# Kernel optimization log

Hardware: AMD Instinct MI355X
Metric: run time of the kernel (lower is better)

## Reference

```python
import jax, jax.numpy as jnp
import numpy as np

ITERS = 10
EPS = 1e-6
TEMPERATURE = 1.0


def setup_inputs() -> dict:
    key = jax.random.key(0)
    S, E = 524288, 64
    logits = jax.random.normal(key, (S, E), dtype=jnp.float32)
    return {"logits": logits, "top_k": 2}


def reference(logits, top_k):
    s, e = logits.shape
    scores = (logits / TEMPERATURE).astype(jnp.float32)
    scores = scores - jnp.max(scores, axis=-1, keepdims=True)
    q = jnp.exp(scores)
    col_target = float(s) / float(max(e, 1))

    def body(q, _):
        q = q / (jnp.sum(q, axis=1, keepdims=True) + EPS)
        q = q / (jnp.sum(q, axis=0, keepdims=True) + EPS) * col_target
        return q, None

    q, _ = jax.lax.scan(body, q, None, length=ITERS)
    q = q / (jnp.sum(q, axis=1, keepdims=True) + EPS)
    vals, idx = jax.lax.top_k(q, top_k)
    w = vals / (jnp.sum(vals, axis=-1, keepdims=True) + EPS)
    return idx.astype(jnp.int64), w.astype(logits.dtype)
```

## Files before the change

kernel.cpp:

```cpp
#include <hip/hip_runtime.h>
#include <math.h>

#define EPS 1e-6f
#define NE 64
#define TPB 1024
#define WPB 16
#define NBLK 256
#define NWAVES (NBLK * WPB)
#define ITERS 10
#define PF 4

template <int ctrl>
__device__ __forceinline__ float dppf(float x) {
    return __int_as_float(__builtin_amdgcn_update_dpp(
        0, __float_as_int(x), ctrl, 0xf, 0xf, true));
}
template <int ctrl>
__device__ __forceinline__ int dppi(int x) {
    return __builtin_amdgcn_update_dpp(0, x, ctrl, 0xf, 0xf, true);
}

__device__ __forceinline__ float group16_sum(float v) {
    v += dppf<0xB1>(v);
    v += dppf<0x4E>(v);
    v += dppf<0x141>(v);
    v += dppf<0x140>(v);
    return v;
}

#define ARGMAX_STEP(CTRL)                                      \
    {                                                          \
        float ov = dppf<CTRL>(v);                              \
        int oi = dppi<CTRL>(i);                                \
        if (ov > v || (ov == v && oi < i)) { v = ov; i = oi; } \
    }

__device__ __forceinline__ void group16_argmax(float& v, int& i) {
    ARGMAX_STEP(0xB1)
    ARGMAX_STEP(0x4E)
    ARGMAX_STEP(0x141)
    ARGMAX_STEP(0x140)
}

__global__ __launch_bounds__(TPB, 4) void sink_fused(
    const float4* __restrict__ logits4,
    float* __restrict__ Pblk,
    unsigned* __restrict__ counters,
    float2* __restrict__ oidx, float2* __restrict__ ow,
    int nquads, float col_target) {
    __shared__ float4 plds[WPB][64];
    __shared__ float s_red[16][NE];
    __shared__ float r_lds[WPB * 128];
    __shared__ float4 c_lds4[NE / 4];

    const int tid = threadIdx.x;
    const int lane = tid & 63;
    const int wib = tid >> 6;
    const int g = lane >> 4;
    const int h = lane & 15;
    const int qpw = nquads / NWAVES;
    const int qbase = (blockIdx.x * WPB + wib) * qpw;
    const float4* lp = logits4 + (size_t)qbase * 64 + lane;
    const int nb = qpw / PF;
    const int lrow0 = wib * 128 + g;

    if (tid < NE / 4) c_lds4[tid] = make_float4(1.f, 1.f, 1.f, 1.f);
    __syncthreads();

    for (int it = 0; it < ITERS; ++it) {
        const float4 c4 = c_lds4[h];
        float* Pcur = Pblk + (size_t)(it & 1) * NBLK * NE;

        float4 buf[PF];
#pragma unroll
        for (int p = 0; p < PF; ++p) buf[p] = lp[(size_t)p * 64];

        float4 pacc = {0.f, 0.f, 0.f, 0.f};
        for (int b = 0; b < nb; ++b) {
            float4 cur[PF];
#pragma unroll
            for (int p = 0; p < PF; ++p) cur[p] = buf[p];
            if (b + 1 < nb) {
                const float4* np = lp + (size_t)(b + 1) * PF * 64;
#pragma unroll
                for (int p = 0; p < PF; ++p) buf[p] = np[(size_t)p * 64];
            }
#pragma unroll
            for (int p = 0; p < PF; ++p) {
                float4 q;
                q.x = __expf(cur[p].x); q.y = __expf(cur[p].y);
                q.z = __expf(cur[p].z); q.w = __expf(cur[p].w);
                float s = q.x * c4.x + q.y * c4.y + q.z * c4.z + q.w * c4.w;
                s = group16_sum(s);
                const int lrow = lrow0 + (b * PF + p) * 4;
                float rold = (it == 0) ? 1.0f : r_lds[lrow];
                float rnew = rold / (rold * s + EPS);
                if (h == 0) r_lds[lrow] = rnew;
                pacc.x += q.x * rnew; pacc.y += q.y * rnew;
                pacc.z += q.z * rnew; pacc.w += q.w * rnew;
            }
        }

        plds[wib][lane] = pacc;
        __syncthreads();
        if (tid < NE) {
            const int hh = tid >> 2, kk = tid & 3;
            float t = 0.f;
#pragma unroll
            for (int w = 0; w < WPB; ++w)
#pragma unroll
                for (int gg = 0; gg < 4; ++gg)
                    t += ((const float*)&plds[w][gg * 16 + hh])[kk];
            __hip_atomic_store(&Pcur[blockIdx.x * NE + tid], t,
                               __ATOMIC_RELAXED, __HIP_MEMORY_SCOPE_AGENT);
        }
        __syncthreads();

        if (tid == 0) {
            __builtin_amdgcn_fence(__ATOMIC_RELEASE, "agent");
            __hip_atomic_fetch_add(&counters[it], 1u, __ATOMIC_RELAXED,
                                   __HIP_MEMORY_SCOPE_AGENT);
            while (__hip_atomic_load(&counters[it], __ATOMIC_RELAXED,
                                     __HIP_MEMORY_SCOPE_AGENT) < (unsigned)NBLK)
                __builtin_amdgcn_s_sleep(2);
            __builtin_amdgcn_fence(__ATOMIC_ACQUIRE, "agent");
        }
        __syncthreads();

        {
            const int col = tid & 63;
            const int chunk = tid >> 6;
            const int b0 = chunk * (NBLK / 16);
            float t = 0.f;
#pragma unroll
            for (int b2 = 0; b2 < NBLK / 16; ++b2)
                t += __hip_atomic_load(&Pcur[(b0 + b2) * NE + col],
                                       __ATOMIC_RELAXED,
                                       __HIP_MEMORY_SCOPE_AGENT);
            s_red[chunk][col] = t;
        }
        __syncthreads();
        if (tid < NE) {
            float P = 0.f;
#pragma unroll
            for (int k = 0; k < 16; ++k) P += s_red[k][tid];
            float cj = ((float*)c_lds4)[tid];
            ((float*)c_lds4)[tid] = cj * col_target / (cj * P + EPS);
        }
        __syncthreads();
    }

    {
        const float4 c4 = c_lds4[h];
        const int base_col = h * 4;

        float4 buf[PF];
#pragma unroll
        for (int p = 0; p < PF; ++p) buf[p] = lp[(size_t)p * 64];

        for (int b = 0; b < nb; ++b) {
            float4 cur[PF];
#pragma unroll
            for (int p = 0; p < PF; ++p) cur[p] = buf[p];
            if (b + 1 < nb) {
                const float4* np = lp + (size_t)(b + 1) * PF * 64;
#pragma unroll
                for (int p = 0; p < PF; ++p) buf[p] = np[(size_t)p * 64];
            }
#pragma unroll
            for (int p = 0; p < PF; ++p) {
                float4 u;
                u.x = __expf(cur[p].x) * c4.x; u.y = __expf(cur[p].y) * c4.y;
                u.z = __expf(cur[p].z) * c4.z; u.w = __expf(cur[p].w) * c4.w;
                float s = group16_sum(u.x + u.y + u.z + u.w);
                const int lrow = lrow0 + (b * PF + p) * 4;
                float rold = r_lds[lrow];
                float rnew = rold / (rold * s + EPS);
                float4 val;
                val.x = u.x * rnew; val.y = u.y * rnew;
                val.z = u.z * rnew; val.w = u.w * rnew;

                float v = val.x; int i = base_col;
                if (val.y > v) { v = val.y; i = base_col + 1; }
                if (val.z > v) { v = val.z; i = base_col + 2; }
                if (val.w > v) { v = val.w; i = base_col + 3; }
                group16_argmax(v, i);
                float v1 = v; int i1 = i;

                float4 mv;
                mv.x = (i1 == base_col)     ? -INFINITY : val.x;
                mv.y = (i1 == base_col + 1) ? -INFINITY : val.y;
                mv.z = (i1 == base_col + 2) ? -INFINITY : val.z;
                mv.w = (i1 == base_col + 3) ? -INFINITY : val.w;
                v = mv.x; i = base_col;
                if (mv.y > v) { v = mv.y; i = base_col + 1; }
                if (mv.z > v) { v = mv.z; i = base_col + 2; }
                if (mv.w > v) { v = mv.w; i = base_col + 3; }
                group16_argmax(v, i);
                float v2 = v; int i2 = i;

                if (h == 0) {
                    int row = (qbase + b * PF + p) * 4 + g;
                    float wsum = v1 + v2 + EPS;
                    oidx[row] = make_float2((float)i1, (float)i2);
                    ow[row] = make_float2(v1 / wsum, v2 / wsum);
                }
            }
        }
    }
}

extern "C" void kernel_launch(void* const* d_in, const int* in_sizes, int n_in,
                              void* d_out, int out_size, void* d_ws, size_t ws_size,
                              hipStream_t stream) {
    const float* logits = (const float*)d_in[0];
    const int S = in_sizes[0] / NE;
    const int nquads = S / 4;
    const float col_target = (float)S / (float)NE;

    float* Pblk = (float*)d_ws;
    unsigned* counters = (unsigned*)(Pblk + 2 * NBLK * NE);

    float* out = (float*)d_out;
    float2* oidx = (float2*)out;
    float2* ow = (float2*)(out + (size_t)2 * S);

    hipMemsetAsync(counters, 0, ITERS * sizeof(unsigned), stream);
    sink_fused<<<NBLK, TPB, 0, stream>>>((const float4*)logits, Pblk, counters,
                                         oidx, ow, nquads, col_target);
}
```

Measured before the change: 555.9 us.

## Deepen prefetch to 8 quads and carry prefetched loads across iteration barriers

Doubles the per-wave software prefetch depth from 4 to 8 float4 loads and rotates the buffer slot by slot, so each slot is refilled right after it is consumed. The last batch of each pass wraps around to prefetch the first batch of the next pass, so loads for the next iteration are in flight during the grid-wide barrier and column reduction. This aims to hide global-memory latency and the per-pass restart bubble. The cost is more VGPRs per thread, which under launch_bounds(1024,4) could cause spills.

```diff
diff --git a/kernel.cpp b/kernel.cpp
--- a/kernel.cpp
+++ b/kernel.cpp
@@ -8,7 +8,7 @@
 #define NBLK 256
 #define NWAVES (NBLK * WPB)
 #define ITERS 10
-#define PF 4
+#define PF 8
 
 template <int ctrl>
 __device__ __forceinline__ float dppf(float x) {
@@ -65,31 +65,27 @@
     const int lrow0 = wib * 128 + g;
 
     if (tid < NE / 4) c_lds4[tid] = make_float4(1.f, 1.f, 1.f, 1.f);
+
+    float4 buf[PF];
+#pragma unroll
+    for (int p = 0; p < PF; ++p) buf[p] = lp[(size_t)p * 64];
     __syncthreads();
 
     for (int it = 0; it < ITERS; ++it) {
         const float4 c4 = c_lds4[h];
         float* Pcur = Pblk + (size_t)(it & 1) * NBLK * NE;
 
-        float4 buf[PF];
-#pragma unroll
-        for (int p = 0; p < PF; ++p) buf[p] = lp[(size_t)p * 64];
-
         float4 pacc = {0.f, 0.f, 0.f, 0.f};
         for (int b = 0; b < nb; ++b) {
-            float4 cur[PF];
-#pragma unroll
-            for (int p = 0; p < PF; ++p) cur[p] = buf[p];
-            if (b + 1 < nb) {
-                const float4* np = lp + (size_t)(b + 1) * PF * 64;
-#pragma unroll
-                for (int p = 0; p < PF; ++p) buf[p] = np[(size_t)p * 64];
-            }
+            const int nxt = (b + 1 < nb) ? (b + 1) * PF : 0;
+            const float4* np = lp + (size_t)nxt * 64;
 #pragma unroll
             for (int p = 0; p < PF; ++p) {
+                const float4 cur = buf[p];
+                buf[p] = np[(size_t)p * 64];
                 float4 q;
-                q.x = __expf(cur[p].x); q.y = __expf(cur[p].y);
-                q.z = __expf(cur[p].z); q.w = __expf(cur[p].w);
+                q.x = __expf(cur.x); q.y = __expf(cur.y);
+                q.z = __expf(cur.z); q.w = __expf(cur.w);
                 float s = q.x * c4.x + q.y * c4.y + q.z * c4.z + q.w * c4.w;
                 s = group16_sum(s);
                 const int lrow = lrow0 + (b * PF + p) * 4;
@@ -154,24 +150,16 @@
         const float4 c4 = c_lds4[h];
         const int base_col = h * 4;
 
-        float4 buf[PF];
-#pragma unroll
-        for (int p = 0; p < PF; ++p) buf[p] = lp[(size_t)p * 64];
-
         for (int b = 0; b < nb; ++b) {
-            float4 cur[PF];
-#pragma unroll
-            for (int p = 0; p < PF; ++p) cur[p] = buf[p];
-            if (b + 1 < nb) {
-                const float4* np = lp + (size_t)(b + 1) * PF * 64;
-#pragma unroll
-                for (int p = 0; p < PF; ++p) buf[p] = np[(size_t)p * 64];
-            }
+            const bool more = (b + 1 < nb);
+            const float4* np = lp + (size_t)(b + 1) * PF * 64;
 #pragma unroll
             for (int p = 0; p < PF; ++p) {
+                const float4 cur = buf[p];
+                if (more) buf[p] = np[(size_t)p * 64];
                 float4 u;
-                u.x = __expf(cur[p].x) * c4.x; u.y = __expf(cur[p].y) * c4.y;
-                u.z = __expf(cur[p].z) * c4.z; u.w = __expf(cur[p].w) * c4.w;
+                u.x = __expf(cur.x) * c4.x; u.y = __expf(cur.y) * c4.y;
+                u.z = __expf(cur.z) * c4.z; u.w = __expf(cur.w) * c4.w;
                 float s = group16_sum(u.x + u.y + u.z + u.w);
                 const int lrow = lrow0 + (b * PF + p) * 4;
                 float rold = r_lds[lrow];
```

Measured after the change: 537.3 us. -3.3%, faster.

## Cache exponentiated logits in registers and LDS across Sinkhorn iterations

Applied to the files above, without the earlier changes.

Each wave's 32 row-quads of exp(logits) are now computed once. The first 16 are kept in registers and the next 8 in dynamic LDS. Only the last 8 are reloaded from global memory and re-exponentiated on each iteration and in the final top-2 pass. This removes most of the repeated 128MB global reads and exp work per iteration. In exchange, register pressure rises, 128KB of dynamic LDS is needed, QPW is hardcoded to 32 so the kernel only handles this problem size, and the occupancy hint is dropped.

```diff
diff --git a/kernel.cpp b/kernel.cpp
--- a/kernel.cpp
+++ b/kernel.cpp
@@ -8,7 +8,10 @@
 #define NBLK 256
 #define NWAVES (NBLK * WPB)
 #define ITERS 10
-#define PF 4
+#define QPW 32
+#define NR 16
+#define NL 8
+#define NS 8
 
 template <int ctrl>
 __device__ __forceinline__ float dppf(float x) {
@@ -42,12 +45,13 @@
     ARGMAX_STEP(0x140)
 }
 
-__global__ __launch_bounds__(TPB, 4) void sink_fused(
+__global__ __launch_bounds__(TPB) void sink_fused(
     const float4* __restrict__ logits4,
     float* __restrict__ Pblk,
     unsigned* __restrict__ counters,
     float2* __restrict__ oidx, float2* __restrict__ ow,
     int nquads, float col_target) {
+    extern __shared__ float4 ldsq[];
     __shared__ float4 plds[WPB][64];
     __shared__ float s_red[16][NE];
     __shared__ float r_lds[WPB * 128];
@@ -58,49 +62,34 @@
     const int wib = tid >> 6;
     const int g = lane >> 4;
     const int h = lane & 15;
-    const int qpw = nquads / NWAVES;
-    const int qbase = (blockIdx.x * WPB + wib) * qpw;
+    const int qbase = (blockIdx.x * WPB + wib) * QPW;
     const float4* lp = logits4 + (size_t)qbase * 64 + lane;
-    const int nb = qpw / PF;
     const int lrow0 = wib * 128 + g;
 
     if (tid < NE / 4) c_lds4[tid] = make_float4(1.f, 1.f, 1.f, 1.f);
     __syncthreads();
 
-    for (int it = 0; it < ITERS; ++it) {
-        const float4 c4 = c_lds4[h];
+    auto exp4 = [](const float4& v) {
+        float4 e;
+        e.x = __expf(v.x); e.y = __expf(v.y);
+        e.z = __expf(v.z); e.w = __expf(v.w);
+        return e;
+    };
+
+    auto procq = [&](const float4& e, int q, const float4& c4, float4& pacc,
+                     bool first) {
+        float s = e.x * c4.x + e.y * c4.y + e.z * c4.z + e.w * c4.w;
+        s = group16_sum(s);
+        const int lrow = lrow0 + q * 4;
+        float rold = first ? 1.0f : r_lds[lrow];
+        float rnew = rold / (rold * s + EPS);
+        if (h == 0) r_lds[lrow] = rnew;
+        pacc.x += e.x * rnew; pacc.y += e.y * rnew;
+        pacc.z += e.z * rnew; pacc.w += e.w * rnew;
+    };
+
+    auto col_reduce_barrier = [&](const float4& pacc, int it) {
         float* Pcur = Pblk + (size_t)(it & 1) * NBLK * NE;
-
-        float4 buf[PF];
-#pragma unroll
-        for (int p = 0; p < PF; ++p) buf[p] = lp[(size_t)p * 64];
-
-        float4 pacc = {0.f, 0.f, 0.f, 0.f};
-        for (int b = 0; b < nb; ++b) {
-            float4 cur[PF];
-#pragma unroll
-            for (int p = 0; p < PF; ++p) cur[p] = buf[p];
-            if (b + 1 < nb) {
-                const float4* np = lp + (size_t)(b + 1) * PF * 64;
-#pragma unroll
-                for (int p = 0; p < PF; ++p) buf[p] = np[(size_t)p * 64];
-            }
-#pragma unroll
-            for (int p = 0; p < PF; ++p) {
-                float4 q;
-                q.x = __expf(cur[p].x); q.y = __expf(cur[p].y);
-                q.z = __expf(cur[p].z); q.w = __expf(cur[p].w);
-                float s = q.x * c4.x + q.y * c4.y + q.z * c4.z + q.w * c4.w;
-                s = group16_sum(s);
-                const int lrow = lrow0 + (b * PF + p) * 4;
-                float rold = (it == 0) ? 1.0f : r_lds[lrow];
-                float rnew = rold / (rold * s + EPS);
-                if (h == 0) r_lds[lrow] = rnew;
-                pacc.x += q.x * rnew; pacc.y += q.y * rnew;
-                pacc.z += q.z * rnew; pacc.w += q.w * rnew;
-            }
-        }
-
         plds[wib][lane] = pacc;
         __syncthreads();
         if (tid < NE) {
@@ -115,7 +104,6 @@
                                __ATOMIC_RELAXED, __HIP_MEMORY_SCOPE_AGENT);
         }
         __syncthreads();
-
         if (tid == 0) {
             __builtin_amdgcn_fence(__ATOMIC_RELEASE, "agent");
             __hip_atomic_fetch_add(&counters[it], 1u, __ATOMIC_RELAXED,
@@ -126,7 +114,6 @@
             __builtin_amdgcn_fence(__ATOMIC_ACQUIRE, "agent");
         }
         __syncthreads();
-
         {
             const int col = tid & 63;
             const int chunk = tid >> 6;
@@ -148,65 +135,135 @@
             ((float*)c_lds4)[tid] = cj * col_target / (cj * P + EPS);
         }
         __syncthreads();
+    };
+
+    float4 RD[NR];
+
+    {
+        const float4 c4 = c_lds4[h];
+        float4 buf[4];
+#pragma unroll
+        for (int p = 0; p < 4; ++p) buf[p] = lp[(size_t)p * 64];
+        float4 pacc = {0.f, 0.f, 0.f, 0.f};
+#pragma unroll
+        for (int b = 0; b < 8; ++b) {
+            float4 cur[4];
+#pragma unroll
+            for (int p = 0; p < 4; ++p) cur[p] = buf[p];
+            if (b < 7) {
+#pragma unroll
+                for (int p = 0; p < 4; ++p)
+                    buf[p] = lp[(size_t)((b + 1) * 4 + p) * 64];
+            }
+#pragma unroll
+            for (int p = 0; p < 4; ++p) {
+                const int q = b * 4 + p;
+                float4 e = exp4(cur[p]);
+                if (q < NR) RD[q] = e;
+                else if (q < NR + NL)
+                    ldsq[(wib * NL + (q - NR)) * 64 + lane] = e;
+                procq(e, q, c4, pacc, true);
+            }
+        }
+        col_reduce_barrier(pacc, 0);
+    }
+
+    for (int it = 1; it < ITERS; ++it) {
+        const float4 c4 = c_lds4[h];
+        float4 sbuf[4];
+#pragma unroll
+        for (int p = 0; p < 4; ++p) sbuf[p] = lp[(size_t)(24 + p) * 64];
+
+        float4 pacc = {0.f, 0.f, 0.f, 0.f};
+#pragma unroll
+        for (int q = 0; q < NR; ++q) procq(RD[q], q, c4, pacc, false);
+
+        float4 sbuf2[4];
+#pragma unroll
+        for (int p = 0; p < 4; ++p) sbuf2[p] = lp[(size_t)(28 + p) * 64];
+
+        float4 lcur = ldsq[(wib * NL) * 64 + lane];
+#pragma unroll
+        for (int j = 0; j < NL; ++j) {
+            float4 lnxt;
+            if (j + 1 < NL) lnxt = ldsq[(wib * NL + j + 1) * 64 + lane];
+            procq(lcur, NR + j, c4, pacc, false);
+            lcur = lnxt;
+        }
+#pragma unroll
+        for (int p = 0; p < 4; ++p) procq(exp4(sbuf[p]), 24 + p, c4, pacc, false);
+#pragma unroll
+        for (int p = 0; p < 4; ++p) procq(exp4(sbuf2[p]), 28 + p, c4, pacc, false);
+
+        col_reduce_barrier(pacc, it);
     }
 
     {
         const float4 c4 = c_lds4[h];
         const int base_col = h * 4;
 
-        float4 buf[PF];
-#pragma unroll
-        for (int p = 0; p < PF; ++p) buf[p] = lp[(size_t)p * 64];
-
-        for (int b = 0; b < nb; ++b) {
-            float4 cur[PF];
-#pragma unroll
-            for (int p = 0; p < PF; ++p) cur[p] = buf[p];
-            if (b + 1 < nb) {
-                const float4* np = lp + (size_t)(b + 1) * PF * 64;
-#pragma unroll
-                for (int p = 0; p < PF; ++p) buf[p] = np[(size_t)p * 64];
+        auto top2 = [&](const float4& e, int q) {
+            float4 u;
+            u.x = e.x * c4.x; u.y = e.y * c4.y;
+            u.z = e.z * c4.z; u.w = e.w * c4.w;
+            float s = group16_sum(u.x + u.y + u.z + u.w);
+            const int lrow = lrow0 + q * 4;
+            float rold = r_lds[lrow];
+            float rnew = rold / (rold * s + EPS);
+            float4 val;
+            val.x = u.x * rnew; val.y = u.y * rnew;
+            val.z = u.z * rnew; val.w = u.w * rnew;
+
+            float v = val.x; int i = base_col;
+            if (val.y > v) { v = val.y; i = base_col + 1; }
+            if (val.z > v) { v = val.z; i = base_col + 2; }
+            if (val.w > v) { v = val.w; i = base_col + 3; }
+            group16_argmax(v, i);
+            float v1 = v; int i1 = i;
+
+            float4 mv;
+            mv.x = (i1 == base_col)     ? -INFINITY : val.x;
+            mv.y = (i1 == base_col + 1) ? -INFINITY : val.y;
+            mv.z = (i1 == base_col + 2) ? -INFINITY : val.z;
+            mv.w = (i1 == base_col + 3) ? -INFINITY : val.w;
+            v = mv.x; i = base_col;
+            if (mv.y > v) { v = mv.y; i = base_col + 1; }
+            if (mv.z > v) { v = mv.z; i = base_col + 2; }
+            if (mv.w > v) { v = mv.w; i = base_col + 3; }
+            group16_argmax(v, i);
+            float v2 = v; int i2 = i;
+
+            if (h == 0) {
+                int row = (qbase + q) * 4 + g;
+                float wsum = v1 + v2 + EPS;
+                oidx[row] = make_float2((float)i1, (float)i2);
+                ow[row] = make_float2(v1 / wsum, v2 / wsum);
             }
-#pragma unroll
-            for (int p = 0; p < PF; ++p) {
-                float4 u;
-                u.x = __expf(cur[p].x) * c4.x; u.y = __expf(cur[p].y) * c4.y;
-                u.z = __expf(cur[p].z) * c4.z; u.w = __expf(cur[p].w) * c4.w;
-                float s = group16_sum(u.x + u.y + u.z + u.w);
-                const int lrow = lrow0 + (b * PF + p) * 4;
-                float rold = r_lds[lrow];
-                float rnew = rold / (rold * s + EPS);
-                float4 val;
-                val.x = u.x * rnew; val.y = u.y * rnew;
-                val.z = u.z * rnew; val.w = u.w * rnew;
-
-                float v = val.x; int i = base_col;
-                if (val.y > v) { v = val.y; i = base_col + 1; }
-                if (val.z > v) { v = val.z; i = base_col + 2; }
-                if (val.w > v) { v = val.w; i = base_col + 3; }
-                group16_argmax(v, i);
-                float v1 = v; int i1 = i;
-
-                float4 mv;
-                mv.x = (i1 == base_col)     ? -INFINITY : val.x;
-                mv.y = (i1 == base_col + 1) ? -INFINITY : val.y;
-                mv.z = (i1 == base_col + 2) ? -INFINITY : val.z;
-                mv.w = (i1 == base_col + 3) ? -INFINITY : val.w;
-                v = mv.x; i = base_col;
-                if (mv.y > v) { v = mv.y; i = base_col + 1; }
-                if (mv.z > v) { v = mv.z; i = base_col + 2; }
-                if (mv.w > v) { v = mv.w; i = base_col + 3; }
-                group16_argmax(v, i);
-                float v2 = v; int i2 = i;
-
-                if (h == 0) {
-                    int row = (qbase + b * PF + p) * 4 + g;
-                    float wsum = v1 + v2 + EPS;
-                    oidx[row] = make_float2((float)i1, (float)i2);
-                    ow[row] = make_float2(v1 / wsum, v2 / wsum);
-                }
-            }
-        }
+        };
+
+        float4 sbuf[4];
+#pragma unroll
+        for (int p = 0; p < 4; ++p) sbuf[p] = lp[(size_t)(24 + p) * 64];
+
+#pragma unroll
+        for (int q = 0; q < NR; ++q) top2(RD[q], q);
+
+        float4 sbuf2[4];
+#pragma unroll
+        for (int p = 0; p < 4; ++p) sbuf2[p] = lp[(size_t)(28 + p) * 64];
+
+        float4 lcur = ldsq[(wib * NL) * 64 + lane];
+#pragma unroll
+        for (int j = 0; j < NL; ++j) {
+            float4 lnxt;
+            if (j + 1 < NL) lnxt = ldsq[(wib * NL + j + 1) * 64 + lane];
+            top2(lcur, NR + j);
+            lcur = lnxt;
+        }
+#pragma unroll
+        for (int p = 0; p < 4; ++p) top2(exp4(sbuf[p]), 24 + p);
+#pragma unroll
+        for (int p = 0; p < 4; ++p) top2(exp4(sbuf2[p]), 28 + p);
     }
 }
 
@@ -225,7 +282,17 @@
     float2* oidx = (float2*)out;
     float2* ow = (float2*)(out + (size_t)2 * S);
 
+    const size_t dyn_lds = (size_t)WPB * NL * 64 * sizeof(float4);
+    static bool attr_done = false;
+    if (!attr_done) {
+        hipFuncSetAttribute(reinterpret_cast<const void*>(sink_fused),
+                            hipFuncAttributeMaxDynamicSharedMemorySize,
+                            (int)dyn_lds);
+        attr_done = true;
+    }
+
     hipMemsetAsync(counters, 0, ITERS * sizeof(unsigned), stream);
-    sink_fused<<<NBLK, TPB, 0, stream>>>((const float4*)logits, Pblk, counters,
-                                         oidx, ow, nquads, col_target);
-}
+    sink_fused<<<NBLK, TPB, dyn_lds, stream>>>((const float4*)logits, Pblk,
+                                               counters, oidx, ow, nquads,
+                                               col_target);
+}
```

Result: slower. 671.3 us (+20.8%).
